# Kernel tuning notes

Hardware: AMD Instinct MI355X
Metric: run time of the kernel (lower is better)

The kernel has to match this reference:

```python
import jax, jax.numpy as jnp
import numpy as np

B = 4
N_TOTAL = 40000
N_SRC0, N_DST0, E0 = 30000, 15000, 360000
N_DST1, E1 = 7500, 180000
D_IN, OUT = 64, 32
H1, C1 = 8, 8
H2, C2 = 1, OUT
NEG_SLOPE = 0.2


def setup_inputs() -> dict:
    key = jax.random.key(0)
    ks = jax.random.split(key, 16)
    inp = {
        'x': jax.random.normal(ks[0], (B, N_TOTAL, D_IN), dtype=jnp.float32),
        'n_id0': jax.random.randint(ks[1], (N_SRC0,), 0, N_SRC0),
        'res_n_id0': jax.random.randint(ks[2], (N_DST0,), 0, N_SRC0),
        'edge_src0': jax.random.randint(ks[3], (E0,), 0, N_SRC0),
        'edge_dst0': jax.random.randint(ks[4], (E0,), 0, N_DST0),
        'res_n_id1': jax.random.randint(ks[5], (N_DST1,), 0, N_DST0),
        'edge_src1': jax.random.randint(ks[6], (E1,), 0, N_DST0),
        'edge_dst1': jax.random.randint(ks[7], (E1,), 0, N_DST1),
        # GATConv params (Glorot-ish scale)
        'W1': jax.random.normal(ks[8], (D_IN, H1 * C1), dtype=jnp.float32) / np.sqrt(D_IN),
        'att_src1': jax.random.normal(ks[9], (H1, C1), dtype=jnp.float32) / np.sqrt(C1),
        'att_dst1': jax.random.normal(ks[10], (H1, C1), dtype=jnp.float32) / np.sqrt(C1),
        'b1': jnp.zeros((H1 * C1,), dtype=jnp.float32),
        'W2': jax.random.normal(ks[11], (H1 * C1, H2 * C2), dtype=jnp.float32) / np.sqrt(H1 * C1),
        'att_src2': jax.random.normal(ks[12], (H2, C2), dtype=jnp.float32) / np.sqrt(C2),
        'att_dst2': jax.random.normal(ks[13], (H2, C2), dtype=jnp.float32) / np.sqrt(C2),
        'b2': jnp.zeros((H2 * C2,), dtype=jnp.float32),
    }
    return inp


def gat_conv(x_src, x_dst, src, dst, W, a_src, a_dst, bias, n_dst, H, C):
    """Bipartite PyG-style GATConv (concat=True, eval mode, no self-loops)."""
    b = x_src.shape[0]
    hs = (x_src @ W).reshape(b, -1, H, C)            # [B, Ns, H, C]
    hd = (x_dst @ W).reshape(b, -1, H, C)            # [B, Nd, H, C]
    es = jnp.einsum('bnhc,hc->bnh', hs, a_src)       # [B, Ns, H]
    ed = jnp.einsum('bnhc,hc->bnh', hd, a_dst)       # [B, Nd, H]
    e = jax.nn.leaky_relu(es[:, src] + ed[:, dst], NEG_SLOPE)  # [B, E, H]
    eT = jnp.swapaxes(e, 0, 1)                       # [E, B, H] (segment over axis 0)
    m = jax.ops.segment_max(eT, dst, num_segments=n_dst)
    p = jnp.exp(eT - m[dst])
    den = jax.ops.segment_sum(p, dst, num_segments=n_dst)
    alpha = p / den[dst]                             # [E, B, H]
    msg = alpha[..., None] * jnp.swapaxes(hs[:, src], 0, 1)    # [E, B, H, C]
    out = jax.ops.segment_sum(msg, dst, num_segments=n_dst)    # [Nd, B, H, C]
    out = jnp.swapaxes(out, 0, 1).reshape(b, n_dst, H * C)
    return out + bias


def reference(x, n_id0, res_n_id0, edge_src0, edge_dst0, res_n_id1, edge_src1,
              edge_dst1, W1, att_src1, att_dst1, b1, W2, att_src2, att_dst2, b2):
    xt = x[:, n_id0, :]                                        # [B, N_SRC0, D_IN]
    h = gat_conv(xt, xt[:, res_n_id0, :], edge_src0, edge_dst0,
                 W1, att_src1, att_dst1, b1, N_DST0, H1, C1)
    h = jax.nn.elu(h)                                          # dropout = identity (eval)
    out = gat_conv(h, h[:, res_n_id1, :], edge_src1, edge_dst1,
                   W2, att_src2, att_dst2, b2, N_DST1, H2, C2)
    return out                                                 # [B, N_DST1, OUT]
```

## Files before the change

### kernel.cpp

```cpp
#include <hip/hip_runtime.h>

#define NB 4
#define NT 40000
#define NS0 30000
#define ND0 15000
#define NE0 360000
#define ND1 7500
#define NE1 180000
#define NEG 0.2f

#define CAP 64
#define K1B ((NB*NS0)/64)
#define SB8 ((NE0 + NE1 + 2047)/2048)

typedef __attribute__((ext_vector_type(8))) short bf8;
typedef __attribute__((ext_vector_type(4))) float f4;

__device__ __forceinline__ unsigned short f2bf(float f) {
    unsigned u = __float_as_uint(f);
    u += 0x7FFF + ((u >> 16) & 1);
    return (unsigned short)(u >> 16);
}
__device__ __forceinline__ float bf_lo(unsigned u) { return __uint_as_float(u << 16); }
__device__ __forceinline__ float bf_hi(unsigned u) { return __uint_as_float(u & 0xFFFF0000u); }

__global__ __launch_bounds__(256) void kA_gemm_scat(
        const float* __restrict__ x, const int* __restrict__ n_id0,
        const float* __restrict__ W1, const float* __restrict__ a_src,
        const float* __restrict__ a_dst,
        unsigned short* __restrict__ ht1b, float* __restrict__ es1, float* __restrict__ ed1,
        const int* __restrict__ esrc0, const int* __restrict__ edst0,
        const int* __restrict__ esrc1, const int* __restrict__ edst1,
        int* __restrict__ cur0, int* __restrict__ cur1,
        int* __restrict__ srcsort0, int* __restrict__ srcsort1) {
    __shared__ unsigned short xtb[64*72];
    __shared__ unsigned short wtb[64*72];
    __shared__ float asl[64], adl[64];
    if (blockIdx.x >= K1B) {
        int base = (blockIdx.x - K1B) * 2048 + threadIdx.x;
        #pragma unroll
        for (int p = 0; p < 8; ++p) {
            int t = base + p * 256;
            if (t < NE0) {
                int d = edst0[t];
                int pos = atomicAdd(&cur0[d], 1);
                if (pos < CAP) srcsort0[d*CAP + pos] = esrc0[t];
            } else if (t < NE0 + NE1) {
                int e = t - NE0;
                int d = edst1[e];
                int pos = atomicAdd(&cur1[d], 1);
                if (pos < CAP) srcsort1[d*CAP + pos] = esrc1[e];
            }
        }
        return;
    }
    int bid = blockIdx.x;
    int t = threadIdx.x;
    {
        int k = t >> 2, nb = (t & 3) * 16;
        const float* wrow = &W1[k*64 + nb];
        #pragma unroll
        for (int j = 0; j < 16; j += 4) {
            float4 v = *(const float4*)&wrow[j];
            wtb[(nb+j+0)*72 + k] = f2bf(v.x);
            wtb[(nb+j+1)*72 + k] = f2bf(v.y);
            wtb[(nb+j+2)*72 + k] = f2bf(v.z);
            wtb[(nb+j+3)*72 + k] = f2bf(v.w);
        }
    }
    if (t < 64) { asl[t] = a_src[t]; adl[t] = a_dst[t]; }
    {
        int r   = t >> 2;
        int sub = t & 3;
        int row_s = bid * 64 + r;
        int bs = row_s / NS0;
        int ns = row_s - bs * NS0;
        const float* xrow = x + ((size_t)(bs * NT + n_id0[ns])) * 64;
        #pragma unroll
        for (int j = 0; j < 4; ++j) {
            int kf = (sub + j*4) * 4;
            float4 v = *(const float4*)&xrow[kf];
            ushort4 u;
            u.x = f2bf(v.x); u.y = f2bf(v.y); u.z = f2bf(v.z); u.w = f2bf(v.w);
            *(ushort4*)&xtb[r*72 + kf] = u;
        }
    }
    __syncthreads();
    int w = t >> 6, lane = t & 63, quad = lane >> 4, cl = lane & 15;
    int arow = 16*w + cl;
    bf8 a0 = *(const bf8*)&xtb[arow*72 + quad*8];
    bf8 a1 = *(const bf8*)&xtb[arow*72 + 32 + quad*8];
    f4 acc[4];
    #pragma unroll
    for (int sub = 0; sub < 4; ++sub) {
        int n = sub*16 + cl;
        bf8 b0 = *(const bf8*)&wtb[n*72 + quad*8];
        bf8 b1v = *(const bf8*)&wtb[n*72 + 32 + quad*8];
        f4 c = {0.f, 0.f, 0.f, 0.f};
        c = __builtin_amdgcn_mfma_f32_16x16x32_bf16(a0, b0, c, 0, 0, 0);
        c = __builtin_amdgcn_mfma_f32_16x16x32_bf16(a1, b1v, c, 0, 0, 0);
        acc[sub] = c;
    }
    int rbase = bid*64 + 16*w + quad*4;
    #pragma unroll
    for (int sub = 0; sub < 4; ++sub)
        #pragma unroll
        for (int r = 0; r < 4; ++r)
            ht1b[(size_t)(rbase + r)*64 + sub*16 + cl] = f2bf(acc[sub][r]);
    #pragma unroll
    for (int r = 0; r < 4; ++r) {
        #pragma unroll
        for (int sub = 0; sub < 4; ++sub) {
            int col = sub*16 + cl;
            float ps = acc[sub][r] * asl[col];
            float pd = acc[sub][r] * adl[col];
            ps += __shfl_xor(ps, 1); ps += __shfl_xor(ps, 2); ps += __shfl_xor(ps, 4);
            pd += __shfl_xor(pd, 1); pd += __shfl_xor(pd, 2); pd += __shfl_xor(pd, 4);
            if ((cl & 7) == 0) {
                int h = sub*2 + (cl >> 3);
                es1[(rbase + r)*8 + h] = ps;
                ed1[(rbase + r)*8 + h] = pd;
            }
        }
    }
}

__global__ __launch_bounds__(256) void k3_agg1_node2(
        const int* __restrict__ srcsort0, const int* __restrict__ cur0,
        const int* __restrict__ res0,
        const float* __restrict__ es1, const float* __restrict__ ed1,
        const unsigned short* __restrict__ ht1b, const float* __restrict__ b1,
        const float* __restrict__ W2, const float* __restrict__ a_src2,
        const float* __restrict__ a_dst2,
        float* __restrict__ ht2, float* __restrict__ es2, float* __restrict__ ed2) {
    __shared__ float W2t[32][68];
    __shared__ float as2[32], ad2[32];
    __shared__ float b1l[64];
    __shared__ float hsh[4][64];
    int t = threadIdx.x;
    {
        float4 v0 = *(const float4*)&W2[t*8];
        float4 v1 = *(const float4*)&W2[t*8 + 4];
        int k = t >> 2, c = (t & 3) * 8;
        W2t[c+0][k] = v0.x; W2t[c+1][k] = v0.y; W2t[c+2][k] = v0.z; W2t[c+3][k] = v0.w;
        W2t[c+4][k] = v1.x; W2t[c+5][k] = v1.y; W2t[c+6][k] = v1.z; W2t[c+7][k] = v1.w;
    }
    if (t < 32) { as2[t] = a_src2[t]; ad2[t] = a_dst2[t]; }
    if (t < 64) b1l[t] = b1[t];
    __syncthreads();
    int xcd = blockIdx.x & 7;
    int b = xcd >> 1;
    int chunk = (blockIdx.x >> 3) * 2 + (xcd & 1);
    int wv = t >> 6;
    int d = chunk * 4 + wv;
    int lane = t & 63;
    int grp = lane >> 3;
    int c = lane & 7;
    int dn = res0[d];
    float edv = ed1[(b*NS0 + dn)*8 + c];
    int start = d * CAP;
    int cnt = cur0[d];
    const float* esb = es1 + (size_t)b*NS0*8;
    const unsigned short* htb = ht1b + (size_t)b*NS0*64;
    float acc[8] = {};
    float wsum = 0.f;
    int i = grp;
    bool v0 = i      < cnt, v1 = i + 8  < cnt,
         v2 = i + 16 < cnt, v3 = i + 24 < cnt;
    int s0 = v0 ? srcsort0[start + i]      : 0;
    int s1 = v1 ? srcsort0[start + i + 8]  : 0;
    int s2 = v2 ? srcsort0[start + i + 16] : 0;
    int s3 = v3 ? srcsort0[start + i + 24] : 0;
    for (;;) {
        float e0 = esb[s0*8 + c], e1 = esb[s1*8 + c];
        float e2 = esb[s2*8 + c], e3 = esb[s3*8 + c];
        uint4 h0 = *(const uint4*)&htb[(size_t)s0*64 + c*8];
        uint4 h1 = *(const uint4*)&htb[(size_t)s1*64 + c*8];
        uint4 h2 = *(const uint4*)&htb[(size_t)s2*64 + c*8];
        uint4 h3 = *(const uint4*)&htb[(size_t)s3*64 + c*8];
        int ni = i + 32;
        bool nv0 = false, nv1 = false, nv2 = false, nv3 = false;
        int t0 = 0, t1 = 0, t2 = 0, t3 = 0;
        if (ni < cnt) {
            nv0 = true;            nv1 = ni + 8  < cnt;
            nv2 = ni + 16 < cnt;   nv3 = ni + 24 < cnt;
            t0 =       srcsort0[start + ni];
            t1 = nv1 ? srcsort0[start + ni + 8]  : 0;
            t2 = nv2 ? srcsort0[start + ni + 16] : 0;
            t3 = nv3 ? srcsort0[start + ni + 24] : 0;
        }
        e0 += edv; e1 += edv; e2 += edv; e3 += edv;
        e0 = e0 > 0.f ? e0 : NEG * e0;
        e1 = e1 > 0.f ? e1 : NEG * e1;
        e2 = e2 > 0.f ? e2 : NEG * e2;
        e3 = e3 > 0.f ? e3 : NEG * e3;
        float w0 = v0 ? __expf(e0) : 0.f;
        float w1 = v1 ? __expf(e1) : 0.f;
        float w2 = v2 ? __expf(e2) : 0.f;
        float w3 = v3 ? __expf(e3) : 0.f;
        acc[0] = fmaf(w0, bf_lo(h0.x), acc[0]); acc[1] = fmaf(w0, bf_hi(h0.x), acc[1]);
        acc[2] = fmaf(w0, bf_lo(h0.y), acc[2]); acc[3] = fmaf(w0, bf_hi(h0.y), acc[3]);
        acc[4] = fmaf(w0, bf_lo(h0.z), acc[4]); acc[5] = fmaf(w0, bf_hi(h0.z), acc[5]);
        acc[6] = fmaf(w0, bf_lo(h0.w), acc[6]); acc[7] = fmaf(w0, bf_hi(h0.w), acc[7]);
        acc[0] = fmaf(w1, bf_lo(h1.x), acc[0]); acc[1] = fmaf(w1, bf_hi(h1.x), acc[1]);
        acc[2] = fmaf(w1, bf_lo(h1.y), acc[2]); acc[3] = fmaf(w1, bf_hi(h1.y), acc[3]);
        acc[4] = fmaf(w1, bf_lo(h1.z), acc[4]); acc[5] = fmaf(w1, bf_hi(h1.z), acc[5]);
        acc[6] = fmaf(w1, bf_lo(h1.w), acc[6]); acc[7] = fmaf(w1, bf_hi(h1.w), acc[7]);
        acc[0] = fmaf(w2, bf_lo(h2.x), acc[0]); acc[1] = fmaf(w2, bf_hi(h2.x), acc[1]);
        acc[2] = fmaf(w2, bf_lo(h2.y), acc[2]); acc[3] = fmaf(w2, bf_hi(h2.y), acc[3]);
        acc[4] = fmaf(w2, bf_lo(h2.z), acc[4]); acc[5] = fmaf(w2, bf_hi(h2.z), acc[5]);
        acc[6] = fmaf(w2, bf_lo(h2.w), acc[6]); acc[7] = fmaf(w2, bf_hi(h2.w), acc[7]);
        acc[0] = fmaf(w3, bf_lo(h3.x), acc[0]); acc[1] = fmaf(w3, bf_hi(h3.x), acc[1]);
        acc[2] = fmaf(w3, bf_lo(h3.y), acc[2]); acc[3] = fmaf(w3, bf_hi(h3.y), acc[3]);
        acc[4] = fmaf(w3, bf_lo(h3.z), acc[4]); acc[5] = fmaf(w3, bf_hi(h3.z), acc[5]);
        acc[6] = fmaf(w3, bf_lo(h3.w), acc[6]); acc[7] = fmaf(w3, bf_hi(h3.w), acc[7]);
        wsum += (w0 + w1) + (w2 + w3);
        i = ni; s0 = t0; s1 = t1; s2 = t2; s3 = t3;
        v0 = nv0; v1 = nv1; v2 = nv2; v3 = nv3;
        if (i >= cnt) break;
    }
    int g0 = grp & 1, g1 = (grp >> 1) & 1, g2 = grp >> 2;
    float n0, n1, n2, n3;
    {
        float s, r;
        s = g0 ? acc[0] : acc[1]; r = __shfl_xor(s, 8);  n0 = (g0 ? acc[1] : acc[0]) + r;
        s = g0 ? acc[2] : acc[3]; r = __shfl_xor(s, 8);  n1 = (g0 ? acc[3] : acc[2]) + r;
        s = g0 ? acc[4] : acc[5]; r = __shfl_xor(s, 8);  n2 = (g0 ? acc[5] : acc[4]) + r;
        s = g0 ? acc[6] : acc[7]; r = __shfl_xor(s, 8);  n3 = (g0 ? acc[7] : acc[6]) + r;
    }
    float m0, m1;
    {
        float s, r;
        s = g1 ? n0 : n1; r = __shfl_xor(s, 16); m0 = (g1 ? n1 : n0) + r;
        s = g1 ? n2 : n3; r = __shfl_xor(s, 16); m1 = (g1 ? n3 : n2) + r;
    }
    float fin;
    {
        float s = g2 ? m0 : m1; float r = __shfl_xor(s, 32); fin = (g2 ? m1 : m0) + r;
    }
    wsum += __shfl_xor(wsum, 8); wsum += __shfl_xor(wsum, 16); wsum += __shfl_xor(wsum, 32);
    float inv = cnt > 0 ? 1.f / wsum : 0.f;
    float o = fin * inv + b1l[(c << 3) | grp];
    o = o > 0.f ? o : __expf(o) - 1.f;
    hsh[wv][(c << 3) | grp] = o;
    int c2 = lane & 31, half = lane >> 5;
    const float4* hp = (const float4*)&hsh[wv][half * 32];
    const float4* wp = (const float4*)&W2t[c2][half * 32];
    float acc2 = 0.f;
    #pragma unroll
    for (int q = 0; q < 8; ++q) {
        float4 hv = hp[q];
        float4 w4 = wp[q];
        acc2 = fmaf(hv.x, w4.x, acc2); acc2 = fmaf(hv.y, w4.y, acc2);
        acc2 = fmaf(hv.z, w4.z, acc2); acc2 = fmaf(hv.w, w4.w, acc2);
    }
    acc2 += __shfl_xor(acc2, 32);
    float ps = acc2 * as2[c2];
    float pd = acc2 * ad2[c2];
    ps += __shfl_xor(ps, 1); ps += __shfl_xor(ps, 2); ps += __shfl_xor(ps, 4);
    ps += __shfl_xor(ps, 8); ps += __shfl_xor(ps, 16);
    pd += __shfl_xor(pd, 1); pd += __shfl_xor(pd, 2); pd += __shfl_xor(pd, 4);
    pd += __shfl_xor(pd, 8); pd += __shfl_xor(pd, 16);
    int row = b*ND0 + d;
    if (half == 0) ht2[(size_t)row*32 + c2] = acc2;
    if (lane == 0) { es2[row] = ps; ed2[row] = pd; }
}

__global__ __launch_bounds__(256) void k7_agg2(
        const int* __restrict__ srcsort1, const int* __restrict__ cur1,
        const int* __restrict__ res1,
        const float* __restrict__ es2, const float* __restrict__ ed2,
        const float* __restrict__ ht2, const float* __restrict__ b2,
        float* __restrict__ outp) {
    int xcd = blockIdx.x & 7;
    int b = xcd >> 1;
    int chunk = (blockIdx.x >> 3) * 2 + (xcd & 1);
    if (chunk >= ND1/4) return;
    int d = chunk * 4 + (threadIdx.x >> 6);
    int lane = threadIdx.x & 63;
    int grp = lane >> 3;
    int c = lane & 7;
    int dn = res1[d];
    float edv = ed2[b*ND0 + dn];
    int start = d * CAP;
    int cnt = cur1[d];
    const float* esb = es2 + (size_t)b*ND0;
    const float* htb = ht2 + (size_t)b*ND0*32;
    float ax = 0.f, ay = 0.f, az = 0.f, aw = 0.f, wsum = 0.f;
    int i = grp;
    bool v0 = i      < cnt, v1 = i + 8  < cnt,
         v2 = i + 16 < cnt, v3 = i + 24 < cnt;
    int s0 = v0 ? srcsort1[start + i]      : 0;
    int s1 = v1 ? srcsort1[start + i + 8]  : 0;
    int s2 = v2 ? srcsort1[start + i + 16] : 0;
    int s3 = v3 ? srcsort1[start + i + 24] : 0;
    for (;;) {
        float lg0 = esb[s0], lg1 = esb[s1], lg2 = esb[s2], lg3 = esb[s3];
        float4 h0 = *(const float4*)&htb[(size_t)s0*32 + c*4];
        float4 h1 = *(const float4*)&htb[(size_t)s1*32 + c*4];
        float4 h2 = *(const float4*)&htb[(size_t)s2*32 + c*4];
        float4 h3 = *(const float4*)&htb[(size_t)s3*32 + c*4];
        int ni = i + 32;
        bool nv0 = false, nv1 = false, nv2 = false, nv3 = false;
        int t0 = 0, t1 = 0, t2 = 0, t3 = 0;
        if (ni < cnt) {
            nv0 = true;            nv1 = ni + 8  < cnt;
            nv2 = ni + 16 < cnt;   nv3 = ni + 24 < cnt;
            t0 =       srcsort1[start + ni];
            t1 = nv1 ? srcsort1[start + ni + 8]  : 0;
            t2 = nv2 ? srcsort1[start + ni + 16] : 0;
            t3 = nv3 ? srcsort1[start + ni + 24] : 0;
        }
        lg0 += edv; lg1 += edv; lg2 += edv; lg3 += edv;
        lg0 = lg0 > 0.f ? lg0 : NEG * lg0;
        lg1 = lg1 > 0.f ? lg1 : NEG * lg1;
        lg2 = lg2 > 0.f ? lg2 : NEG * lg2;
        lg3 = lg3 > 0.f ? lg3 : NEG * lg3;
        float w0 = v0 ? __expf(lg0) : 0.f;
        float w1 = v1 ? __expf(lg1) : 0.f;
        float w2 = v2 ? __expf(lg2) : 0.f;
        float w3 = v3 ? __expf(lg3) : 0.f;
        ax = fmaf(w0, h0.x, ax); ay = fmaf(w0, h0.y, ay);
        az = fmaf(w0, h0.z, az); aw = fmaf(w0, h0.w, aw);
        ax = fmaf(w1, h1.x, ax); ay = fmaf(w1, h1.y, ay);
        az = fmaf(w1, h1.z, az); aw = fmaf(w1, h1.w, aw);
        ax = fmaf(w2, h2.x, ax); ay = fmaf(w2, h2.y, ay);
        az = fmaf(w2, h2.z, az); aw = fmaf(w2, h2.w, aw);
        ax = fmaf(w3, h3.x, ax); ay = fmaf(w3, h3.y, ay);
        az = fmaf(w3, h3.z, az); aw = fmaf(w3, h3.w, aw);
        wsum += (w0 + w1) + (w2 + w3);
        i = ni; s0 = t0; s1 = t1; s2 = t2; s3 = t3;
        v0 = nv0; v1 = nv1; v2 = nv2; v3 = nv3;
        if (i >= cnt) break;
    }
    ax += __shfl_xor(ax, 8); ax += __shfl_xor(ax, 16); ax += __shfl_xor(ax, 32);
    ay += __shfl_xor(ay, 8); ay += __shfl_xor(ay, 16); ay += __shfl_xor(ay, 32);
    az += __shfl_xor(az, 8); az += __shfl_xor(az, 16); az += __shfl_xor(az, 32);
    aw += __shfl_xor(aw, 8); aw += __shfl_xor(aw, 16); aw += __shfl_xor(aw, 32);
    wsum += __shfl_xor(wsum, 8); wsum += __shfl_xor(wsum, 16); wsum += __shfl_xor(wsum, 32);
    if (grp == 0) {
        float inv = cnt > 0 ? 1.f / wsum : 0.f;
        float4 bb = *(const float4*)&b2[c*4];
        float4 o;
        o.x = ax*inv + bb.x; o.y = ay*inv + bb.y;
        o.z = az*inv + bb.z; o.w = aw*inv + bb.w;
        *(float4*)&outp[((size_t)(b*ND1 + d))*32 + c*4] = o;
    }
}

extern "C" void kernel_launch(void* const* d_in, const int* in_sizes, int n_in,
                              void* d_out, int out_size, void* d_ws, size_t ws_size,
                              hipStream_t stream) {
    const float* x        = (const float*)d_in[0];
    const int*   n_id0    = (const int*)d_in[1];
    const int*   res0     = (const int*)d_in[2];
    const int*   esrc0    = (const int*)d_in[3];
    const int*   edst0    = (const int*)d_in[4];
    const int*   res1     = (const int*)d_in[5];
    const int*   esrc1    = (const int*)d_in[6];
    const int*   edst1    = (const int*)d_in[7];
    const float* W1       = (const float*)d_in[8];
    const float* a_src1   = (const float*)d_in[9];
    const float* a_dst1   = (const float*)d_in[10];
    const float* b1       = (const float*)d_in[11];
    const float* W2       = (const float*)d_in[12];
    const float* a_src2   = (const float*)d_in[13];
    const float* a_dst2   = (const float*)d_in[14];
    const float* b2       = (const float*)d_in[15];
    float* outp = (float*)d_out;

    char* base = (char*)d_ws;
    unsigned short* ht1b = (unsigned short*)base;
    float* es1  = (float*)(base + 15360000);
    float* ed1  = es1 + 960000;
    float* ht2  = ed1 + 960000;
    float* es2  = ht2 + 1920000;
    float* ed2  = es2 + 60000;
    int* cur0     = (int*)(ed2 + 60000);
    int* cur1     = cur0 + ND0;
    int* srcsort0 = cur1 + ND1;
    int* srcsort1 = srcsort0 + ND0*CAP;

    hipMemsetAsync(cur0, 0, (ND0 + ND1) * sizeof(int), stream);
    kA_gemm_scat<<<K1B + SB8, 256, 0, stream>>>(x, n_id0, W1, a_src1, a_dst1,
                                                ht1b, es1, ed1,
                                                esrc0, edst0, esrc1, edst1,
                                                cur0, cur1, srcsort0, srcsort1);
    k3_agg1_node2<<<NB*(ND0/4), 256, 0, stream>>>(srcsort0, cur0, res0, es1, ed1, ht1b, b1,
                                                  W2, a_src2, a_dst2, ht2, es2, ed2);
    k7_agg2<<<7504, 256, 0, stream>>>(srcsort1, cur1, res1, es2, ed2, ht2, b2, outp);
}
```

Baseline: 191.6 us.

## Interleave es/ed arrays, stage GEMM output via LDS, use persistent grid-stride aggregation

Attention source and destination scores are stored interleaved (es,ed pairs) so each producer writes one float2 instead of two scattered floats. The first GEMM's bf16 output is staged through shared memory and written back as coalesced 16-byte rows instead of strided 2-byte stores. Both aggregation kernels become grid-stride loops over 2048 blocks instead of one block per chunk, which cuts block launch overhead and lets the per-block W2 setup be reused across chunks. The trade-offs are an extra sync and LDS pass in the GEMM, and interleaved scores that halve the useful bytes per cache line on the source-score gathers.

```diff
diff --git a/kernel.cpp b/kernel.cpp
--- a/kernel.cpp
+++ b/kernel.cpp
@@ -28,7 +28,7 @@
         const float* __restrict__ x, const int* __restrict__ n_id0,
         const float* __restrict__ W1, const float* __restrict__ a_src,
         const float* __restrict__ a_dst,
-        unsigned short* __restrict__ ht1b, float* __restrict__ es1, float* __restrict__ ed1,
+        unsigned short* __restrict__ ht1b, float* __restrict__ esd1,
         const int* __restrict__ esrc0, const int* __restrict__ edst0,
         const int* __restrict__ esrc1, const int* __restrict__ edst1,
         int* __restrict__ cur0, int* __restrict__ cur1,
@@ -101,12 +101,14 @@
         c = __builtin_amdgcn_mfma_f32_16x16x32_bf16(a1, b1v, c, 0, 0, 0);
         acc[sub] = c;
     }
-    int rbase = bid*64 + 16*w + quad*4;
+    __syncthreads();
+    unsigned short* ob = xtb;
     #pragma unroll
     for (int sub = 0; sub < 4; ++sub)
         #pragma unroll
         for (int r = 0; r < 4; ++r)
-            ht1b[(size_t)(rbase + r)*64 + sub*16 + cl] = f2bf(acc[sub][r]);
+            ob[(16*w + 4*quad + r)*64 + sub*16 + cl] = f2bf(acc[sub][r]);
+    int rbase = bid*64 + 16*w + quad*4;
     #pragma unroll
     for (int r = 0; r < 4; ++r) {
         #pragma unroll
@@ -118,9 +120,19 @@
             pd += __shfl_xor(pd, 1); pd += __shfl_xor(pd, 2); pd += __shfl_xor(pd, 4);
             if ((cl & 7) == 0) {
                 int h = sub*2 + (cl >> 3);
-                es1[(rbase + r)*8 + h] = ps;
-                ed1[(rbase + r)*8 + h] = pd;
+                *(float2*)&esd1[(size_t)(rbase + r)*16 + h*2] = make_float2(ps, pd);
             }
+        }
+    }
+    __syncthreads();
+    {
+        int row = t >> 3;
+        int c8  = t & 7;
+        #pragma unroll
+        for (int rep = 0; rep < 2; ++rep) {
+            int rr2 = row + rep*32;
+            uint4 v = *(const uint4*)&ob[rr2*64 + c8*8];
+            *(uint4*)&ht1b[((size_t)(bid*64 + rr2))*64 + c8*8] = v;
         }
     }
 }
@@ -128,11 +140,11 @@
 __global__ __launch_bounds__(256) void k3_agg1_node2(
         const int* __restrict__ srcsort0, const int* __restrict__ cur0,
         const int* __restrict__ res0,
-        const float* __restrict__ es1, const float* __restrict__ ed1,
+        const float* __restrict__ esd1,
         const unsigned short* __restrict__ ht1b, const float* __restrict__ b1,
         const float* __restrict__ W2, const float* __restrict__ a_src2,
         const float* __restrict__ a_dst2,
-        float* __restrict__ ht2, float* __restrict__ es2, float* __restrict__ ed2) {
+        float* __restrict__ ht2, float* __restrict__ esd2) {
     __shared__ float W2t[32][68];
     __shared__ float as2[32], ad2[32];
     __shared__ float b1l[64];
@@ -150,201 +162,205 @@
     __syncthreads();
     int xcd = blockIdx.x & 7;
     int b = xcd >> 1;
-    int chunk = (blockIdx.x >> 3) * 2 + (xcd & 1);
+    int pb2 = (blockIdx.x >> 3) * 2 + (xcd & 1);
     int wv = t >> 6;
-    int d = chunk * 4 + wv;
     int lane = t & 63;
     int grp = lane >> 3;
     int c = lane & 7;
-    int dn = res0[d];
-    float edv = ed1[(b*NS0 + dn)*8 + c];
-    int start = d * CAP;
-    int cnt = cur0[d];
-    const float* esb = es1 + (size_t)b*NS0*8;
+    const float* esb = esd1 + (size_t)b*NS0*16;
     const unsigned short* htb = ht1b + (size_t)b*NS0*64;
-    float acc[8] = {};
-    float wsum = 0.f;
-    int i = grp;
-    bool v0 = i      < cnt, v1 = i + 8  < cnt,
-         v2 = i + 16 < cnt, v3 = i + 24 < cnt;
-    int s0 = v0 ? srcsort0[start + i]      : 0;
-    int s1 = v1 ? srcsort0[start + i + 8]  : 0;
-    int s2 = v2 ? srcsort0[start + i + 16] : 0;
-    int s3 = v3 ? srcsort0[start + i + 24] : 0;
-    for (;;) {
-        float e0 = esb[s0*8 + c], e1 = esb[s1*8 + c];
-        float e2 = esb[s2*8 + c], e3 = esb[s3*8 + c];
-        uint4 h0 = *(const uint4*)&htb[(size_t)s0*64 + c*8];
-        uint4 h1 = *(const uint4*)&htb[(size_t)s1*64 + c*8];
-        uint4 h2 = *(const uint4*)&htb[(size_t)s2*64 + c*8];
-        uint4 h3 = *(const uint4*)&htb[(size_t)s3*64 + c*8];
-        int ni = i + 32;
-        bool nv0 = false, nv1 = false, nv2 = false, nv3 = false;
-        int t0 = 0, t1 = 0, t2 = 0, t3 = 0;
-        if (ni < cnt) {
-            nv0 = true;            nv1 = ni + 8  < cnt;
-            nv2 = ni + 16 < cnt;   nv3 = ni + 24 < cnt;
-            t0 =       srcsort0[start + ni];
-            t1 = nv1 ? srcsort0[start + ni + 8]  : 0;
-            t2 = nv2 ? srcsort0[start + ni + 16] : 0;
-            t3 = nv3 ? srcsort0[start + ni + 24] : 0;
-        }
-        e0 += edv; e1 += edv; e2 += edv; e3 += edv;
-        e0 = e0 > 0.f ? e0 : NEG * e0;
-        e1 = e1 > 0.f ? e1 : NEG * e1;
-        e2 = e2 > 0.f ? e2 : NEG * e2;
-        e3 = e3 > 0.f ? e3 : NEG * e3;
-        float w0 = v0 ? __expf(e0) : 0.f;
-        float w1 = v1 ? __expf(e1) : 0.f;
-        float w2 = v2 ? __expf(e2) : 0.f;
-        float w3 = v3 ? __expf(e3) : 0.f;
-        acc[0] = fmaf(w0, bf_lo(h0.x), acc[0]); acc[1] = fmaf(w0, bf_hi(h0.x), acc[1]);
-        acc[2] = fmaf(w0, bf_lo(h0.y), acc[2]); acc[3] = fmaf(w0, bf_hi(h0.y), acc[3]);
-        acc[4] = fmaf(w0, bf_lo(h0.z), acc[4]); acc[5] = fmaf(w0, bf_hi(h0.z), acc[5]);
-        acc[6] = fmaf(w0, bf_lo(h0.w), acc[6]); acc[7] = fmaf(w0, bf_hi(h0.w), acc[7]);
-        acc[0] = fmaf(w1, bf_lo(h1.x), acc[0]); acc[1] = fmaf(w1, bf_hi(h1.x), acc[1]);
-        acc[2] = fmaf(w1, bf_lo(h1.y), acc[2]); acc[3] = fmaf(w1, bf_hi(h1.y), acc[3]);
-        acc[4] = fmaf(w1, bf_lo(h1.z), acc[4]); acc[5] = fmaf(w1, bf_hi(h1.z), acc[5]);
-        acc[6] = fmaf(w1, bf_lo(h1.w), acc[6]); acc[7] = fmaf(w1, bf_hi(h1.w), acc[7]);
-        acc[0] = fmaf(w2, bf_lo(h2.x), acc[0]); acc[1] = fmaf(w2, bf_hi(h2.x), acc[1]);
-        acc[2] = fmaf(w2, bf_lo(h2.y), acc[2]); acc[3] = fmaf(w2, bf_hi(h2.y), acc[3]);
-        acc[4] = fmaf(w2, bf_lo(h2.z), acc[4]); acc[5] = fmaf(w2, bf_hi(h2.z), acc[5]);
-        acc[6] = fmaf(w2, bf_lo(h2.w), acc[6]); acc[7] = fmaf(w2, bf_hi(h2.w), acc[7]);
-        acc[0] = fmaf(w3, bf_lo(h3.x), acc[0]); acc[1] = fmaf(w3, bf_hi(h3.x), acc[1]);
-        acc[2] = fmaf(w3, bf_lo(h3.y), acc[2]); acc[3] = fmaf(w3, bf_hi(h3.y), acc[3]);
-        acc[4] = fmaf(w3, bf_lo(h3.z), acc[4]); acc[5] = fmaf(w3, bf_hi(h3.z), acc[5]);
-        acc[6] = fmaf(w3, bf_lo(h3.w), acc[6]); acc[7] = fmaf(w3, bf_hi(h3.w), acc[7]);
-        wsum += (w0 + w1) + (w2 + w3);
-        i = ni; s0 = t0; s1 = t1; s2 = t2; s3 = t3;
-        v0 = nv0; v1 = nv1; v2 = nv2; v3 = nv3;
-        if (i >= cnt) break;
-    }
-    int g0 = grp & 1, g1 = (grp >> 1) & 1, g2 = grp >> 2;
-    float n0, n1, n2, n3;
-    {
-        float s, r;
-        s = g0 ? acc[0] : acc[1]; r = __shfl_xor(s, 8);  n0 = (g0 ? acc[1] : acc[0]) + r;
-        s = g0 ? acc[2] : acc[3]; r = __shfl_xor(s, 8);  n1 = (g0 ? acc[3] : acc[2]) + r;
-        s = g0 ? acc[4] : acc[5]; r = __shfl_xor(s, 8);  n2 = (g0 ? acc[5] : acc[4]) + r;
-        s = g0 ? acc[6] : acc[7]; r = __shfl_xor(s, 8);  n3 = (g0 ? acc[7] : acc[6]) + r;
-    }
-    float m0, m1;
-    {
-        float s, r;
-        s = g1 ? n0 : n1; r = __shfl_xor(s, 16); m0 = (g1 ? n1 : n0) + r;
-        s = g1 ? n2 : n3; r = __shfl_xor(s, 16); m1 = (g1 ? n3 : n2) + r;
-    }
-    float fin;
-    {
-        float s = g2 ? m0 : m1; float r = __shfl_xor(s, 32); fin = (g2 ? m1 : m0) + r;
-    }
-    wsum += __shfl_xor(wsum, 8); wsum += __shfl_xor(wsum, 16); wsum += __shfl_xor(wsum, 32);
-    float inv = cnt > 0 ? 1.f / wsum : 0.f;
-    float o = fin * inv + b1l[(c << 3) | grp];
-    o = o > 0.f ? o : __expf(o) - 1.f;
-    hsh[wv][(c << 3) | grp] = o;
-    int c2 = lane & 31, half = lane >> 5;
-    const float4* hp = (const float4*)&hsh[wv][half * 32];
-    const float4* wp = (const float4*)&W2t[c2][half * 32];
-    float acc2 = 0.f;
-    #pragma unroll
-    for (int q = 0; q < 8; ++q) {
-        float4 hv = hp[q];
-        float4 w4 = wp[q];
-        acc2 = fmaf(hv.x, w4.x, acc2); acc2 = fmaf(hv.y, w4.y, acc2);
-        acc2 = fmaf(hv.z, w4.z, acc2); acc2 = fmaf(hv.w, w4.w, acc2);
-    }
-    acc2 += __shfl_xor(acc2, 32);
-    float ps = acc2 * as2[c2];
-    float pd = acc2 * ad2[c2];
-    ps += __shfl_xor(ps, 1); ps += __shfl_xor(ps, 2); ps += __shfl_xor(ps, 4);
-    ps += __shfl_xor(ps, 8); ps += __shfl_xor(ps, 16);
-    pd += __shfl_xor(pd, 1); pd += __shfl_xor(pd, 2); pd += __shfl_xor(pd, 4);
-    pd += __shfl_xor(pd, 8); pd += __shfl_xor(pd, 16);
-    int row = b*ND0 + d;
-    if (half == 0) ht2[(size_t)row*32 + c2] = acc2;
-    if (lane == 0) { es2[row] = ps; ed2[row] = pd; }
+    for (int chunk = pb2; chunk < ND0/4; chunk += 512) {
+        int d = chunk * 4 + wv;
+        int dn = res0[d];
+        float edv = esb[(size_t)dn*16 + c*2 + 1];
+        int start = d * CAP;
+        int cnt = cur0[d];
+        float acc[8] = {};
+        float wsum = 0.f;
+        int i = grp;
+        bool v0 = i      < cnt, v1 = i + 8  < cnt,
+             v2 = i + 16 < cnt, v3 = i + 24 < cnt;
+        int s0 = v0 ? srcsort0[start + i]      : 0;
+        int s1 = v1 ? srcsort0[start + i + 8]  : 0;
+        int s2 = v2 ? srcsort0[start + i + 16] : 0;
+        int s3 = v3 ? srcsort0[start + i + 24] : 0;
+        for (;;) {
+            float e0 = esb[s0*16 + c*2], e1 = esb[s1*16 + c*2];
+            float e2 = esb[s2*16 + c*2], e3 = esb[s3*16 + c*2];
+            uint4 h0 = *(const uint4*)&htb[(size_t)s0*64 + c*8];
+            uint4 h1 = *(const uint4*)&htb[(size_t)s1*64 + c*8];
+            uint4 h2 = *(const uint4*)&htb[(size_t)s2*64 + c*8];
+            uint4 h3 = *(const uint4*)&htb[(size_t)s3*64 + c*8];
+            int ni = i + 32;
+            bool nv0 = false, nv1 = false, nv2 = false, nv3 = false;
+            int t0 = 0, t1 = 0, t2 = 0, t3 = 0;
+            if (ni < cnt) {
+                nv0 = true;            nv1 = ni + 8  < cnt;
+                nv2 = ni + 16 < cnt;   nv3 = ni + 24 < cnt;
+                t0 =       srcsort0[start + ni];
+                t1 = nv1 ? srcsort0[start + ni + 8]  : 0;
+                t2 = nv2 ? srcsort0[start + ni + 16] : 0;
+                t3 = nv3 ? srcsort0[start + ni + 24] : 0;
+            }
+            e0 += edv; e1 += edv; e2 += edv; e3 += edv;
+            e0 = e0 > 0.f ? e0 : NEG * e0;
+            e1 = e1 > 0.f ? e1 : NEG * e1;
+            e2 = e2 > 0.f ? e2 : NEG * e2;
+            e3 = e3 > 0.f ? e3 : NEG * e3;
+            float w0 = v0 ? __expf(e0) : 0.f;
+            float w1 = v1 ? __expf(e1) : 0.f;
+            float w2 = v2 ? __expf(e2) : 0.f;
+            float w3 = v3 ? __expf(e3) : 0.f;
+            acc[0] = fmaf(w0, bf_lo(h0.x), acc[0]); acc[1] = fmaf(w0, bf_hi(h0.x), acc[1]);
+            acc[2] = fmaf(w0, bf_lo(h0.y), acc[2]); acc[3] = fmaf(w0, bf_hi(h0.y), acc[3]);
+            acc[4] = fmaf(w0, bf_lo(h0.z), acc[4]); acc[5] = fmaf(w0, bf_hi(h0.z), acc[5]);
+            acc[6] = fmaf(w0, bf_lo(h0.w), acc[6]); acc[7] = fmaf(w0, bf_hi(h0.w), acc[7]);
+            acc[0] = fmaf(w1, bf_lo(h1.x), acc[0]); acc[1] = fmaf(w1, bf_hi(h1.x), acc[1]);
+            acc[2] = fmaf(w1, bf_lo(h1.y), acc[2]); acc[3] = fmaf(w1, bf_hi(h1.y), acc[3]);
+            acc[4] = fmaf(w1, bf_lo(h1.z), acc[4]); acc[5] = fmaf(w1, bf_hi(h1.z), acc[5]);
+            acc[6] = fmaf(w1, bf_lo(h1.w), acc[6]); acc[7] = fmaf(w1, bf_hi(h1.w), acc[7]);
+            acc[0] = fmaf(w2, bf_lo(h2.x), acc[0]); acc[1] = fmaf(w2, bf_hi(h2.x), acc[1]);
+            acc[2] = fmaf(w2, bf_lo(h2.y), acc[2]); acc[3] = fmaf(w2, bf_hi(h2.y), acc[3]);
+            acc[4] = fmaf(w2, bf_lo(h2.z), acc[4]); acc[5] = fmaf(w2, bf_hi(h2.z), acc[5]);
+            acc[6] = fmaf(w2, bf_lo(h2.w), acc[6]); acc[7] = fmaf(w2, bf_hi(h2.w), acc[7]);
+            acc[0] = fmaf(w3, bf_lo(h3.x), acc[0]); acc[1] = fmaf(w3, bf_hi(h3.x), acc[1]);
+            acc[2] = fmaf(w3, bf_lo(h3.y), acc[2]); acc[3] = fmaf(w3, bf_hi(h3.y), acc[3]);
+            acc[4] = fmaf(w3, bf_lo(h3.z), acc[4]); acc[5] = fmaf(w3, bf_hi(h3.z), acc[5]);
+            acc[6] = fmaf(w3, bf_lo(h3.w), acc[6]); acc[7] = fmaf(w3, bf_hi(h3.w), acc[7]);
+            wsum += (w0 + w1) + (w2 + w3);
+            i = ni; s0 = t0; s1 = t1; s2 = t2; s3 = t3;
+            v0 = nv0; v1 = nv1; v2 = nv2; v3 = nv3;
+            if (i >= cnt) break;
+        }
+        int g0 = grp & 1, g1 = (grp >> 1) & 1, g2 = grp >> 2;
+        float n0, n1, n2, n3;
+        {
+            float s, r;
+            s = g0 ? acc[0] : acc[1]; r = __shfl_xor(s, 8);  n0 = (g0 ? acc[1] : acc[0]) + r;
+            s = g0 ? acc[2] : acc[3]; r = __shfl_xor(s, 8);  n1 = (g0 ? acc[3] : acc[2]) + r;
+            s = g0 ? acc[4] : acc[5]; r = __shfl_xor(s, 8);  n2 = (g0 ? acc[5] : acc[4]) + r;
+            s = g0 ? acc[6] : acc[7]; r = __shfl_xor(s, 8);  n3 = (g0 ? acc[7] : acc[6]) + r;
+        }
+        float m0, m1;
+        {
+            float s, r;
+            s = g1 ? n0 : n1; r = __shfl_xor(s, 16); m0 = (g1 ? n1 : n0) + r;
+            s = g1 ? n2 : n3; r = __shfl_xor(s, 16); m1 = (g1 ? n3 : n2) + r;
+        }
+        float fin;
+        {
+            float s = g2 ? m0 : m1; float r = __shfl_xor(s, 32); fin = (g2 ? m1 : m0) + r;
+        }
+        wsum += __shfl_xor(wsum, 8); wsum += __shfl_xor(wsum, 16); wsum += __shfl_xor(wsum, 32);
+        float inv = cnt > 0 ? 1.f / wsum : 0.f;
+        float o = fin * inv + b1l[(c << 3) | grp];
+        o = o > 0.f ? o : __expf(o) - 1.f;
+        hsh[wv][(c << 3) | grp] = o;
+        int c2 = lane & 31, half = lane >> 5;
+        const float4* hp = (const float4*)&hsh[wv][half * 32];
+        const float4* wp = (const float4*)&W2t[c2][half * 32];
+        float acc2 = 0.f;
+        #pragma unroll
+        for (int q = 0; q < 8; ++q) {
+            float4 hv = hp[q];
+            float4 w4 = wp[q];
+            acc2 = fmaf(hv.x, w4.x, acc2); acc2 = fmaf(hv.y, w4.y, acc2);
+            acc2 = fmaf(hv.z, w4.z, acc2); acc2 = fmaf(hv.w, w4.w, acc2);
+        }
+        acc2 += __shfl_xor(acc2, 32);
+        float ps = acc2 * as2[c2];
+        float pd = acc2 * ad2[c2];
+        ps += __shfl_xor(ps, 1); ps += __shfl_xor(ps, 2); ps += __shfl_xor(ps, 4);
+        ps += __shfl_xor(ps, 8); ps += __shfl_xor(ps, 16);
+        pd += __shfl_xor(pd, 1); pd += __shfl_xor(pd, 2); pd += __shfl_xor(pd, 4);
+        pd += __shfl_xor(pd, 8); pd += __shfl_xor(pd, 16);
+        int row = b*ND0 + d;
+        if (half == 0) ht2[(size_t)row*32 + c2] = acc2;
+        if (lane == 0) *(float2*)&esd2[(size_t)row*2] = make_float2(ps, pd);
+    }
 }
 
 __global__ __launch_bounds__(256) void k7_agg2(
         const int* __restrict__ srcsort1, const int* __restrict__ cur1,
         const int* __restrict__ res1,
-        const float* __restrict__ es2, const float* __restrict__ ed2,
+        const float* __restrict__ esd2,
         const float* __restrict__ ht2, const float* __restrict__ b2,
         float* __restrict__ outp) {
     int xcd = blockIdx.x & 7;
     int b = xcd >> 1;
-    int chunk = (blockIdx.x >> 3) * 2 + (xcd & 1);
-    if (chunk >= ND1/4) return;
-    int d = chunk * 4 + (threadIdx.x >> 6);
+    int pb2 = (blockIdx.x >> 3) * 2 + (xcd & 1);
     int lane = threadIdx.x & 63;
+    int wv = threadIdx.x >> 6;
     int grp = lane >> 3;
     int c = lane & 7;
-    int dn = res1[d];
-    float edv = ed2[b*ND0 + dn];
-    int start = d * CAP;
-    int cnt = cur1[d];
-    const float* esb = es2 + (size_t)b*ND0;
+    const float* esb = esd2 + (size_t)b*ND0*2;
     const float* htb = ht2 + (size_t)b*ND0*32;
-    float ax = 0.f, ay = 0.f, az = 0.f, aw = 0.f, wsum = 0.f;
-    int i = grp;
-    bool v0 = i      < cnt, v1 = i + 8  < cnt,
-         v2 = i + 16 < cnt, v3 = i + 24 < cnt;
-    int s0 = v0 ? srcsort1[start + i]      : 0;
-    int s1 = v1 ? srcsort1[start + i + 8]  : 0;
-    int s2 = v2 ? srcsort1[start + i + 16] : 0;
-    int s3 = v3 ? srcsort1[start + i + 24] : 0;
-    for (;;) {
-        float lg0 = esb[s0], lg1 = esb[s1], lg2 = esb[s2], lg3 = esb[s3];
-        float4 h0 = *(const float4*)&htb[(size_t)s0*32 + c*4];
-        float4 h1 = *(const float4*)&htb[(size_t)s1*32 + c*4];
-        float4 h2 = *(const float4*)&htb[(size_t)s2*32 + c*4];
-        float4 h3 = *(const float4*)&htb[(size_t)s3*32 + c*4];
-        int ni = i + 32;
-        bool nv0 = false, nv1 = false, nv2 = false, nv3 = false;
-        int t0 = 0, t1 = 0, t2 = 0, t3 = 0;
-        if (ni < cnt) {
-            nv0 = true;            nv1 = ni + 8  < cnt;
-            nv2 = ni + 16 < cnt;   nv3 = ni + 24 < cnt;
-            t0 =       srcsort1[start + ni];
-            t1 = nv1 ? srcsort1[start + ni + 8]  : 0;
-            t2 = nv2 ? srcsort1[start + ni + 16] : 0;
-            t3 = nv3 ? srcsort1[start + ni + 24] : 0;
-        }
-        lg0 += edv; lg1 += edv; lg2 += edv; lg3 += edv;
-        lg0 = lg0 > 0.f ? lg0 : NEG * lg0;
-        lg1 = lg1 > 0.f ? lg1 : NEG * lg1;
-        lg2 = lg2 > 0.f ? lg2 : NEG * lg2;
-        lg3 = lg3 > 0.f ? lg3 : NEG * lg3;
-        float w0 = v0 ? __expf(lg0) : 0.f;
-        float w1 = v1 ? __expf(lg1) : 0.f;
-        float w2 = v2 ? __expf(lg2) : 0.f;
-        float w3 = v3 ? __expf(lg3) : 0.f;
-        ax = fmaf(w0, h0.x, ax); ay = fmaf(w0, h0.y, ay);
-        az = fmaf(w0, h0.z, az); aw = fmaf(w0, h0.w, aw);
-        ax = fmaf(w1, h1.x, ax); ay = fmaf(w1, h1.y, ay);
-        az = fmaf(w1, h1.z, az); aw = fmaf(w1, h1.w, aw);
-        ax = fmaf(w2, h2.x, ax); ay = fmaf(w2, h2.y, ay);
-        az = fmaf(w2, h2.z, az); aw = fmaf(w2, h2.w, aw);
-        ax = fmaf(w3, h3.x, ax); ay = fmaf(w3, h3.y, ay);
-        az = fmaf(w3, h3.z, az); aw = fmaf(w3, h3.w, aw);
-        wsum += (w0 + w1) + (w2 + w3);
-        i = ni; s0 = t0; s1 = t1; s2 = t2; s3 = t3;
-        v0 = nv0; v1 = nv1; v2 = nv2; v3 = nv3;
-        if (i >= cnt) break;
-    }
-    ax += __shfl_xor(ax, 8); ax += __shfl_xor(ax, 16); ax += __shfl_xor(ax, 32);
-    ay += __shfl_xor(ay, 8); ay += __shfl_xor(ay, 16); ay += __shfl_xor(ay, 32);
-    az += __shfl_xor(az, 8); az += __shfl_xor(az, 16); az += __shfl_xor(az, 32);
-    aw += __shfl_xor(aw, 8); aw += __shfl_xor(aw, 16); aw += __shfl_xor(aw, 32);
-    wsum += __shfl_xor(wsum, 8); wsum += __shfl_xor(wsum, 16); wsum += __shfl_xor(wsum, 32);
-    if (grp == 0) {
-        float inv = cnt > 0 ? 1.f / wsum : 0.f;
-        float4 bb = *(const float4*)&b2[c*4];
-        float4 o;
-        o.x = ax*inv + bb.x; o.y = ay*inv + bb.y;
-        o.z = az*inv + bb.z; o.w = aw*inv + bb.w;
-        *(float4*)&outp[((size_t)(b*ND1 + d))*32 + c*4] = o;
+    for (int chunk = pb2; chunk < ND1/4; chunk += 512) {
+        int d = chunk * 4 + wv;
+        int dn = res1[d];
+        float edv = esb[(size_t)dn*2 + 1];
+        int start = d * CAP;
+        int cnt = cur1[d];
+        float ax = 0.f, ay = 0.f, az = 0.f, aw = 0.f, wsum = 0.f;
+        int i = grp;
+        bool v0 = i      < cnt, v1 = i + 8  < cnt,
+             v2 = i + 16 < cnt, v3 = i + 24 < cnt;
+        int s0 = v0 ? srcsort1[start + i]      : 0;
+        int s1 = v1 ? srcsort1[start + i + 8]  : 0;
+        int s2 = v2 ? srcsort1[start + i + 16] : 0;
+        int s3 = v3 ? srcsort1[start + i + 24] : 0;
+        for (;;) {
+            float lg0 = esb[s0*2], lg1 = esb[s1*2], lg2 = esb[s2*2], lg3 = esb[s3*2];
+            float4 h0 = *(const float4*)&htb[(size_t)s0*32 + c*4];
+            float4 h1 = *(const float4*)&htb[(size_t)s1*32 + c*4];
+            float4 h2 = *(const float4*)&htb[(size_t)s2*32 + c*4];
+            float4 h3 = *(const float4*)&htb[(size_t)s3*32 + c*4];
+            int ni = i + 32;
+            bool nv0 = false, nv1 = false, nv2 = false, nv3 = false;
+            int t0 = 0, t1 = 0, t2 = 0, t3 = 0;
+            if (ni < cnt) {
+                nv0 = true;            nv1 = ni + 8  < cnt;
+                nv2 = ni + 16 < cnt;   nv3 = ni + 24 < cnt;
+                t0 =       srcsort1[start + ni];
+                t1 = nv1 ? srcsort1[start + ni + 8]  : 0;
+                t2 = nv2 ? srcsort1[start + ni + 16] : 0;
+                t3 = nv3 ? srcsort1[start + ni + 24] : 0;
+            }
+            lg0 += edv; lg1 += edv; lg2 += edv; lg3 += edv;
+            lg0 = lg0 > 0.f ? lg0 : NEG * lg0;
+            lg1 = lg1 > 0.f ? lg1 : NEG * lg1;
+            lg2 = lg2 > 0.f ? lg2 : NEG * lg2;
+            lg3 = lg3 > 0.f ? lg3 : NEG * lg3;
+            float w0 = v0 ? __expf(lg0) : 0.f;
+            float w1 = v1 ? __expf(lg1) : 0.f;
+            float w2 = v2 ? __expf(lg2) : 0.f;
+            float w3 = v3 ? __expf(lg3) : 0.f;
+            ax = fmaf(w0, h0.x, ax); ay = fmaf(w0, h0.y, ay);
+            az = fmaf(w0, h0.z, az); aw = fmaf(w0, h0.w, aw);
+            ax = fmaf(w1, h1.x, ax); ay = fmaf(w1, h1.y, ay);
+            az = fmaf(w1, h1.z, az); aw = fmaf(w1, h1.w, aw);
+            ax = fmaf(w2, h2.x, ax); ay = fmaf(w2, h2.y, ay);
+            az = fmaf(w2, h2.z, az); aw = fmaf(w2, h2.w, aw);
+            ax = fmaf(w3, h3.x, ax); ay = fmaf(w3, h3.y, ay);
+            az = fmaf(w3, h3.z, az); aw = fmaf(w3, h3.w, aw);
+            wsum += (w0 + w1) + (w2 + w3);
+            i = ni; s0 = t0; s1 = t1; s2 = t2; s3 = t3;
+            v0 = nv0; v1 = nv1; v2 = nv2; v3 = nv3;
+            if (i >= cnt) break;
+        }
+        ax += __shfl_xor(ax, 8); ax += __shfl_xor(ax, 16); ax += __shfl_xor(ax, 32);
+        ay += __shfl_xor(ay, 8); ay += __shfl_xor(ay, 16); ay += __shfl_xor(ay, 32);
+        az += __shfl_xor(az, 8); az += __shfl_xor(az, 16); az += __shfl_xor(az, 32);
+        aw += __shfl_xor(aw, 8); aw += __shfl_xor(aw, 16); aw += __shfl_xor(aw, 32);
+        wsum += __shfl_xor(wsum, 8); wsum += __shfl_xor(wsum, 16); wsum += __shfl_xor(wsum, 32);
+        if (grp == 0) {
+            float inv = cnt > 0 ? 1.f / wsum : 0.f;
+            float4 bb = *(const float4*)&b2[c*4];
+            float4 o;
+            o.x = ax*inv + bb.x; o.y = ay*inv + bb.y;
+            o.z = az*inv + bb.z; o.w = aw*inv + bb.w;
+            *(float4*)&outp[((size_t)(b*ND1 + d))*32 + c*4] = o;
+        }
     }
 }
 
@@ -371,22 +387,20 @@
 
     char* base = (char*)d_ws;
     unsigned short* ht1b = (unsigned short*)base;
-    float* es1  = (float*)(base + 15360000);
-    float* ed1  = es1 + 960000;
-    float* ht2  = ed1 + 960000;
-    float* es2  = ht2 + 1920000;
-    float* ed2  = es2 + 60000;
-    int* cur0     = (int*)(ed2 + 60000);
+    float* esd1 = (float*)(base + 15360000);
+    float* ht2  = esd1 + 1920000;
+    float* esd2 = ht2 + 1920000;
+    int* cur0     = (int*)(esd2 + 120000);
     int* cur1     = cur0 + ND0;
     int* srcsort0 = cur1 + ND1;
     int* srcsort1 = srcsort0 + ND0*CAP;
 
     hipMemsetAsync(cur0, 0, (ND0 + ND1) * sizeof(int), stream);
     kA_gemm_scat<<<K1B + SB8, 256, 0, stream>>>(x, n_id0, W1, a_src1, a_dst1,
-                                                ht1b, es1, ed1,
+                                                ht1b, esd1,
                                                 esrc0, edst0, esrc1, edst1,
                                                 cur0, cur1, srcsort0, srcsort1);
-    k3_agg1_node2<<<NB*(ND0/4), 256, 0, stream>>>(srcsort0, cur0, res0, es1, ed1, ht1b, b1,
-                                                  W2, a_src2, a_dst2, ht2, es2, ed2);
-    k7_agg2<<<7504, 256, 0, stream>>>(srcsort1, cur1, res1, es2, ed2, ht2, b2, outp);
+    k3_agg1_node2<<<2048, 256, 0, stream>>>(srcsort0, cur0, res0, esd1, ht1b, b1,
+                                            W2, a_src2, a_dst2, ht2, esd2);
+    k7_agg2<<<2048, 256, 0, stream>>>(srcsort1, cur1, res1, esd2, ht2, b2, outp);
 }
```

After: 190.9 us. Within noise of the previous version (-0.4%).
